# Optimization experiments

Hardware: AMD Instinct MI355X
Metric: run time of the kernel (lower is better)

## Reference

```python
import jax, jax.numpy as jnp
import numpy as np

B, P, C, WIN = 64, 24, 40, 64          # batch, acoustic params, phoneme classes, window
L1 = WIN - 4                            # after conv k=5: 60
L2 = L1 - 4                             # after primary conv k=5: 56
R = P * L2                              # num_routes = 24*56 = 1344
IC, OC = 32, 16                         # capsule in/out channels
NUM_ITERS = 3


def squash(x, axis=-1):
    sq = jnp.sum(x * x, axis=axis, keepdims=True)
    return (sq / (1.0 + sq)) * x / (jnp.sqrt(sq) + 1e-8)


def conv1d(x, w, b):
    # x: (B, Cin, L), w: (Cout, Cin, K)
    out = jax.lax.conv_general_dilated(x, w, (1,), 'VALID',
                                       dimension_numbers=('NCH', 'OIH', 'NCH'))
    return out + b[None, :, None]


def batchnorm(x, g, b):
    # training-mode BN over (batch, length) per channel; x: (B, Ch, L)
    m = jnp.mean(x, axis=(0, 2), keepdims=True)
    v = jnp.var(x, axis=(0, 2), keepdims=True)
    return g[None, :, None] * (x - m) / jnp.sqrt(v + 1e-5) + b[None, :, None]


def setup_inputs() -> dict:
    key = jax.random.key(0)
    ks = jax.random.split(key, 12)
    d = {}
    d['x'] = jax.random.normal(ks[0], (B, WIN, P), dtype=jnp.float32)
    # project: Conv1d(24 -> 256, k=5) + BN(256)
    d['conv1_w'] = jax.random.normal(ks[1], (256, P, 5), dtype=jnp.float32) * (1.0 / np.sqrt(P * 5))
    d['conv1_b'] = jnp.zeros((256,), dtype=jnp.float32)
    d['bn1_g'] = jnp.ones((256,), dtype=jnp.float32)
    d['bn1_b'] = jnp.zeros((256,), dtype=jnp.float32)
    d['prim_w'] = jax.random.normal(ks[2], (P * 32, 256, 5), dtype=jnp.float32) * (1.0 / np.sqrt(256 * 5))
    d['prim_b'] = jnp.zeros((P * 32,), dtype=jnp.float32)
    d['bn2_g'] = jnp.ones((32,), dtype=jnp.float32)
    d['bn2_b'] = jnp.zeros((32,), dtype=jnp.float32)
    # digit capsule routing weights (1, C, R, 16, 32) as in torch (randn)
    d['W_cap'] = jax.random.normal(ks[3], (1, C, R, OC, IC), dtype=jnp.float32) * 0.05
    # classifier: Linear(16*C -> 256), Linear(256 -> C)
    d['cls_w1'] = jax.random.normal(ks[4], (256, OC * C), dtype=jnp.float32) * (1.0 / np.sqrt(OC * C))
    d['cls_b1'] = jnp.zeros((256,), dtype=jnp.float32)
    d['cls_w2'] = jax.random.normal(ks[5], (C, 256), dtype=jnp.float32) * (1.0 / np.sqrt(256))
    d['cls_b2'] = jnp.zeros((C,), dtype=jnp.float32)
    d['dec_w1'] = jax.random.normal(ks[6], (256, OC * C), dtype=jnp.float32) * (1.0 / np.sqrt(OC * C))
    d['dec_b1'] = jnp.zeros((256,), dtype=jnp.float32)
    d['dec_w2'] = jax.random.normal(ks[7], (WIN * P, 256), dtype=jnp.float32) * (1.0 / np.sqrt(256))
    d['dec_b2'] = jnp.zeros((WIN * P,), dtype=jnp.float32)
    return d


def reference(x, conv1_w, conv1_b, bn1_g, bn1_b, prim_w, prim_b, bn2_g, bn2_b,
              W_cap, cls_w1, cls_b1, cls_w2, cls_b2, dec_w1, dec_b1, dec_w2, dec_b2):
    h = jax.nn.relu(batchnorm(conv1d(jnp.transpose(x, (0, 2, 1)), conv1_w, conv1_b), bn1_g, bn1_b))
    # primary capsules: fused conv -> (B, 24*32, 56); capsule i occupies length slice i
    u = conv1d(h, prim_w, prim_b)                       # (B, 768, 56)
    u = u.reshape(B, P, 32, L2).transpose(0, 2, 1, 3).reshape(B, 32, R)  # concat along length dim
    u = batchnorm(u, bn2_g, bn2_b)
    u = squash(jnp.transpose(u, (0, 2, 1)), axis=-1)    # (B, R, 32)
    # digit capsule: u_hat = W @ x  -> (B, C, R, 16)
    u_hat = jnp.einsum('crdi,bri->bcrd', W_cap[0], u)
    # dynamic routing
    b_ij = jnp.zeros((B, C, R, 1), dtype=u_hat.dtype)
    for it in range(NUM_ITERS):
        c_ij = jax.nn.softmax(b_ij, axis=1)             # softmax over capsules
        s_j = jnp.sum(c_ij * u_hat, axis=2)             # (B, C, 16)
        v_j = squash(s_j, axis=-1)
        if it < NUM_ITERS - 1:
            a_ij = jnp.einsum('bcrd,bcd->bcr', u_hat, v_j)[..., None]
            b_ij = b_ij + a_ij
    flat = v_j.reshape(B, -1)                           # (B, 640)
    logits = jax.nn.relu(flat @ cls_w1.T + cls_b1) @ cls_w2.T + cls_b2
    pred_y = jax.nn.softmax(logits, axis=-1)
    # y is None branch: one-hot of argmax
    y = jax.nn.one_hot(jnp.argmax(pred_y, axis=1), C, dtype=v_j.dtype)
    masked = (v_j * y[:, :, None]).reshape(B, -1)
    pred_x = jax.nn.sigmoid(jax.nn.relu(masked @ dec_w1.T + dec_b1) @ dec_w2.T + dec_b2)
    pred_x = pred_x.reshape(B, WIN, P)
    return (pred_x, pred_y)
```

## Files before the change

### kernel.cpp

```cpp
#include <hip/hip_runtime.h>
#include <math.h>

#define BB_ 64
#define P_  24
#define C_  40
#define WIN_ 64
#define L1_ 60
#define L2_ 56
#define R_  1344

#define O_USQ   0ull
#define O_UHAT  2752512ull
#define O_H     30277632ull
#define O_HB    3735552ull
#define O_WT    4227072ull
#define O_UP    25755648ull
#define O_STATS 57802752ull
#define O_A1    57803328ull
#define O_B1S   57803584ull
#define O_A2    57803840ull
#define O_B2S   57803872ull
#define O_S     57803904ull
#define O_V     57967744ull
#define WS_FLOATS_NEEDED 58008704ull

typedef short bf16x8 __attribute__((ext_vector_type(8)));
typedef float f32x4 __attribute__((ext_vector_type(4)));

__device__ __forceinline__ float dot4f(float4 a, float4 b) {
    return a.x*b.x + a.y*b.y + a.z*b.z + a.w*b.w;
}

__device__ __forceinline__ unsigned short f2bf(float x) {
    unsigned int u = __float_as_uint(x);
    u += 0x7fffu + ((u >> 16) & 1u);
    return (unsigned short)(u >> 16);
}
__device__ __forceinline__ float bfl(unsigned int u) {
    return __uint_as_float(u << 16);
}
__device__ __forceinline__ float bfh(unsigned int u) {
    return __uint_as_float(u & 0xffff0000u);
}

__global__ void k0w(const float* __restrict__ w2, unsigned short* __restrict__ wt) {
    int o2 = blockIdx.x, t = threadIdx.x;
    const float* src = &w2[(size_t)o2 * 1280 + t * 5];
    #pragma unroll
    for (int kt = 0; kt < 5; kt++)
        wt[((size_t)kt * 768 + o2) * 256 + t] = f2bf(src[kt]);
}

__global__ void k1_conv1(const float* __restrict__ x, const float* __restrict__ w1,
                         const float* __restrict__ c1b, float* __restrict__ h) {
    __shared__ float xs[24 * 20];
    __shared__ float wl[64 * 121];
    int t = threadIdx.x;
    int lq = blockIdx.x, b = blockIdx.y, ocg = blockIdx.z;
    for (int idx = t; idx < 456; idx += 256) {
        int p = idx / 19, tau = idx - p * 19;
        xs[p * 20 + tau] = x[b * 1536 + (lq * 15 + tau) * 24 + p];
    }
    for (int idx = t; idx < 7680; idx += 256) {
        int o_ = idx / 120, cix = idx - o_ * 120;
        wl[o_ * 121 + cix] = w1[(ocg * 64 + o_) * 120 + cix];
    }
    __syncthreads();
    int g = t >> 6;
    int ol = t & 63;
    int LV = (g < 3) ? 4 : 3;
    int o = ocg * 64 + ol;
    float acc[4] = {0.f, 0.f, 0.f, 0.f};
    for (int p = 0; p < 24; p++) {
        float4 xa = *(const float4*)&xs[p * 20 + g * 4];
        float4 xb = *(const float4*)&xs[p * 20 + g * 4 + 4];
        float xr[8] = {xa.x, xa.y, xa.z, xa.w, xb.x, xb.y, xb.z, xb.w};
        #pragma unroll
        for (int k = 0; k < 5; k++) {
            float w = wl[ol * 121 + p * 5 + k];
            #pragma unroll
            for (int li = 0; li < 4; li++) acc[li] += xr[li + k] * w;
        }
    }
    for (int li = 0; li < LV; li++) {
        int l = lq * 15 + g * 4 + li;
        h[(size_t)(b * 60 + l) * 256 + o] = acc[li] + c1b[o];
    }
}

__global__ void k2a(const float* __restrict__ h, float* __restrict__ sum1, float* __restrict__ ss1) {
    int t = threadIdx.x;
    float s = 0.f, q = 0.f;
    for (int i = 0; i < 64; i++) {
        float v = h[(size_t)(blockIdx.x * 64 + i) * 256 + t];
        s += v; q += v * v;
    }
    atomicAdd(&sum1[t], s);
    atomicAdd(&ss1[t], q);
}

__global__ void k2b(const float* __restrict__ sum1, const float* __restrict__ ss1,
                    const float* __restrict__ g, const float* __restrict__ be,
                    float* __restrict__ a1, float* __restrict__ b1s) {
    int o = threadIdx.x;
    float m = sum1[o] * (1.f / 3840.f);
    float v = ss1[o] * (1.f / 3840.f) - m * m;
    float a = g[o] / sqrtf(v + 1e-5f);
    a1[o] = a;
    b1s[o] = be[o] - m * a;
}

__global__ void k2c(const float* __restrict__ h, const float* __restrict__ a1,
                    const float* __restrict__ b1s, unsigned short* __restrict__ hb) {
    int gid = blockIdx.x * 256 + threadIdx.x;
    int base = gid * 4;
    int ic = base & 255;
    float4 v = *(const float4*)&h[base];
    float4 a = *(const float4*)&a1[ic];
    float4 bb = *(const float4*)&b1s[ic];
    unsigned int w0 = (unsigned int)f2bf(fmaxf(v.x * a.x + bb.x, 0.f))
                    | ((unsigned int)f2bf(fmaxf(v.y * a.y + bb.y, 0.f)) << 16);
    unsigned int w1 = (unsigned int)f2bf(fmaxf(v.z * a.z + bb.z, 0.f))
                    | ((unsigned int)f2bf(fmaxf(v.w * a.w + bb.w, 0.f)) << 16);
    uint2 o = {w0, w1};
    *(uint2*)&hb[base] = o;
}

__global__ __launch_bounds__(256) void k3_mfma(
        const unsigned short* __restrict__ hb, const unsigned short* __restrict__ wt,
        const float* __restrict__ pb, float* __restrict__ up) {
    __shared__ unsigned short hs[68 * 40];
    __shared__ unsigned short wsd[5 * 64 * 40];
    int t = threadIdx.x;
    int m0 = blockIdx.x * 64;
    int b = blockIdx.y;
    int wid = t >> 6, lane = t & 63;
    int wm = wid >> 1, wn = wid & 1;
    int ln = lane & 15, grp = lane >> 4;

    f32x4 acc[2][2];
    #pragma unroll
    for (int i = 0; i < 2; i++)
        #pragma unroll
        for (int j = 0; j < 2; j++) acc[i][j] = (f32x4){0.f, 0.f, 0.f, 0.f};

    for (int ic0 = 0; ic0 < 256; ic0 += 32) {
        __syncthreads();
        for (int idx = t; idx < 272; idx += 256) {
            int row = idx >> 2, q = idx & 3;
            int hrow = row < 60 ? row : 59;
            uint4 v = *(const uint4*)&hb[((size_t)b * 60 + hrow) * 256 + ic0 + q * 8];
            *(uint4*)&hs[row * 40 + q * 8] = v;
        }
        #pragma unroll
        for (int it = 0; it < 5; it++) {
            int idx = it * 256 + t;
            int row = idx >> 2, q = idx & 3;
            int kt = row >> 6, o2l = row & 63;
            uint4 v = *(const uint4*)&wt[((size_t)kt * 768 + m0 + o2l) * 256 + ic0 + q * 8];
            *(uint4*)&wsd[row * 40 + q * 8] = v;
        }
        __syncthreads();
        #pragma unroll
        for (int kt = 0; kt < 5; kt++) {
            bf16x8 af0 = *(const bf16x8*)&wsd[(kt * 64 + wm * 32 + ln) * 40 + grp * 8];
            bf16x8 af1 = *(const bf16x8*)&wsd[(kt * 64 + wm * 32 + 16 + ln) * 40 + grp * 8];
            bf16x8 bf0 = *(const bf16x8*)&hs[(wn * 32 + ln + kt) * 40 + grp * 8];
            bf16x8 bf1 = *(const bf16x8*)&hs[(wn * 32 + 16 + ln + kt) * 40 + grp * 8];
            acc[0][0] = __builtin_amdgcn_mfma_f32_16x16x32_bf16(af0, bf0, acc[0][0], 0, 0, 0);
            acc[0][1] = __builtin_amdgcn_mfma_f32_16x16x32_bf16(af0, bf1, acc[0][1], 0, 0, 0);
            acc[1][0] = __builtin_amdgcn_mfma_f32_16x16x32_bf16(af1, bf0, acc[1][0], 0, 0, 0);
            acc[1][1] = __builtin_amdgcn_mfma_f32_16x16x32_bf16(af1, bf1, acc[1][1], 0, 0, 0);
        }
    }
    #pragma unroll
    for (int ms = 0; ms < 2; ms++) {
        int o2 = m0 + wm * 32 + ms * 16 + grp * 4;
        float4 pv = *(const float4*)&pb[o2];
        #pragma unroll
        for (int ns = 0; ns < 2; ns++) {
            int l = wn * 32 + ns * 16 + ln;
            if (l < 56) {
                float4 v;
                v.x = acc[ms][ns][0] + pv.x;
                v.y = acc[ms][ns][1] + pv.y;
                v.z = acc[ms][ns][2] + pv.z;
                v.w = acc[ms][ns][3] + pv.w;
                *(float4*)&up[(size_t)b * 43008 + (size_t)l * 768 + o2] = v;
            }
        }
    }
}

__global__ void k4s(const float* __restrict__ up, float* __restrict__ sum2, float* __restrict__ ss2) {
    __shared__ float rs[256], rq[256];
    int t = threadIdx.x;
    float s = 0.f, q = 0.f;
    for (int i = 0; i < 32; i++) {
        size_t row = (size_t)(blockIdx.x * 32 + i) * 768;
        for (int c0 = 0; c0 < 768; c0 += 256) {
            float v = up[row + c0 + t];
            s += v; q += v * v;
        }
    }
    rs[t] = s; rq[t] = q;
    __syncthreads();
    if (t < 32) {
        float S = 0.f, Q = 0.f;
        for (int g2 = 0; g2 < 8; g2++) { S += rs[t + 32 * g2]; Q += rq[t + 32 * g2]; }
        atomicAdd(&sum2[t], S);
        atomicAdd(&ss2[t], Q);
    }
}

__global__ void k4b(const float* __restrict__ sum2, const float* __restrict__ ss2,
                    const float* __restrict__ g, const float* __restrict__ be,
                    float* __restrict__ a2, float* __restrict__ b2s) {
    int j = threadIdx.x;
    if (j >= 32) return;
    float m = sum2[j] * (1.f / 86016.f);
    float v = ss2[j] * (1.f / 86016.f) - m * m;
    float a = g[j] / sqrtf(v + 1e-5f);
    a2[j] = a;
    b2s[j] = be[j] - m * a;
}

__global__ void k5(const float* __restrict__ up, const float* __restrict__ a2,
                   const float* __restrict__ b2s, float* __restrict__ usq) {
    int t = threadIdx.x;
    int row = blockIdx.x * 8 + (t >> 5);
    int j = t & 31;
    int b = row / 1344, r = row - b * 1344;
    int p = r / 56, l = r - p * 56;
    float v = up[(size_t)b * 43008 + (size_t)l * 768 + p * 32 + j];
    float xv = a2[j] * v + b2s[j];
    float sq = xv * xv;
    #pragma unroll
    for (int m = 16; m >= 1; m >>= 1) sq += __shfl_xor(sq, m, 32);
    float scale = (sq / (1.f + sq)) / (sqrtf(sq) + 1e-8f);
    usq[(size_t)row * 32 + j] = xv * scale;
}

__global__ __launch_bounds__(256) void k6_uhat(const float* __restrict__ usq,
                                               const float* __restrict__ W,
                                               unsigned short* __restrict__ uhb) {
    __shared__ float us[64 * 36];
    __shared__ float wl[128 * 36];
    int t = threadIdx.x;
    int cdt = blockIdx.x, r = blockIdx.y;

    #pragma unroll
    for (int q = 0; q < 2; q++) {
        int idx4 = q * 256 + t;
        int b = idx4 >> 3, i4 = idx4 & 7;
        float4 v = *(const float4*)&usq[(size_t)(b * 1344 + r) * 32 + i4 * 4];
        *(float4*)&us[b * 36 + i4 * 4] = v;
    }
    #pragma unroll
    for (int q = 0; q < 4; q++) {
        int idx4 = q * 256 + t;
        int c_l = idx4 >> 7;
        int rest4 = idx4 & 127;
        float4 v = *(const float4*)&W[(size_t)(cdt * 8 + c_l) * 688128ull +
                                      (size_t)r * 512 + rest4 * 4];
        int cd_l = c_l * 16 + (rest4 >> 3);
        int i4 = rest4 & 7;
        *(float4*)&wl[cd_l * 36 + i4 * 4] = v;
    }
    __syncthreads();

    int tb = t & 7, tcd = t >> 3;
    float acc[8][4];
    #pragma unroll
    for (int i = 0; i < 8; i++)
        #pragma unroll
        for (int j = 0; j < 4; j++) acc[i][j] = 0.f;

    #pragma unroll
    for (int k4 = 0; k4 < 8; k4++) {
        float4 wv[4], ub[8];
        #pragma unroll
        for (int j = 0; j < 4; j++)
            wv[j] = *(const float4*)&wl[(tcd * 4 + j) * 36 + k4 * 4];
        #pragma unroll
        for (int bj = 0; bj < 8; bj++)
            ub[bj] = *(const float4*)&us[(bj * 8 + tb) * 36 + k4 * 4];
        #pragma unroll
        for (int bj = 0; bj < 8; bj++)
            #pragma unroll
            for (int j = 0; j < 4; j++)
                acc[bj][j] += dot4f(ub[bj], wv[j]);
    }

    #pragma unroll
    for (int bj = 0; bj < 8; bj++) {
        int b = bj * 8 + tb;
        unsigned int lo = (unsigned int)f2bf(acc[bj][0]) | ((unsigned int)f2bf(acc[bj][1]) << 16);
        unsigned int hi = (unsigned int)f2bf(acc[bj][2]) | ((unsigned int)f2bf(acc[bj][3]) << 16);
        uint2 o = {lo, hi};
        *(uint2*)&uhb[(size_t)(b * 1344 + r) * 640 + cdt * 128 + tcd * 4] = o;
    }
}

template<int UNIFORM>
__global__ void k_route(const unsigned short* __restrict__ uhb, const float* __restrict__ vsum,
                        float* __restrict__ sout) {
    __shared__ float sl[2560];
    int t = threadIdx.x, wid = t >> 6, lane = t & 63;
    int b = blockIdx.y, rt = blockIdx.x;
    bool act = lane < 40;
    int c = act ? lane : 0;
    float4 vs0 = {0,0,0,0}, vs1 = vs0, vs2 = vs0, vs3 = vs0;
    if (UNIFORM == 0 && act) {
        const float4* vp = (const float4*)&vsum[b * 640 + c * 16];
        vs0 = vp[0]; vs1 = vp[1]; vs2 = vp[2]; vs3 = vp[3];
    }
    float4 ac0 = {0,0,0,0}, ac1 = ac0, ac2 = ac0, ac3 = ac0;
    for (int i = 0; i < 8; i++) {
        int r = rt * 32 + wid * 8 + i;
        const uint4* u4 = (const uint4*)&uhb[((size_t)(b * 1344 + r) * 40 + c) * 16];
        float4 a0 = {0,0,0,0}, a1 = a0, a2 = a0, a3 = a0;
        if (act) {
            uint4 q0 = u4[0], q1 = u4[1];
            a0.x = bfl(q0.x); a0.y = bfh(q0.x); a0.z = bfl(q0.y); a0.w = bfh(q0.y);
            a1.x = bfl(q0.z); a1.y = bfh(q0.z); a1.z = bfl(q0.w); a1.w = bfh(q0.w);
            a2.x = bfl(q1.x); a2.y = bfh(q1.x); a2.z = bfl(q1.y); a2.w = bfh(q1.y);
            a3.x = bfl(q1.z); a3.y = bfh(q1.z); a3.z = bfl(q1.w); a3.w = bfh(q1.w);
        }
        float w;
        if (UNIFORM) {
            w = 0.025f;
        } else {
            float dt = act ? (dot4f(a0, vs0) + dot4f(a1, vs1) + dot4f(a2, vs2) + dot4f(a3, vs3))
                           : -1e30f;
            float mx = dt;
            #pragma unroll
            for (int m2 = 32; m2 >= 1; m2 >>= 1) mx = fmaxf(mx, __shfl_xor(mx, m2));
            float e = act ? __expf(dt - mx) : 0.f;
            float se = e;
            #pragma unroll
            for (int m2 = 32; m2 >= 1; m2 >>= 1) se += __shfl_xor(se, m2);
            w = e / se;
        }
        ac0.x += w * a0.x; ac0.y += w * a0.y; ac0.z += w * a0.z; ac0.w += w * a0.w;
        ac1.x += w * a1.x; ac1.y += w * a1.y; ac1.z += w * a1.z; ac1.w += w * a1.w;
        ac2.x += w * a2.x; ac2.y += w * a2.y; ac2.z += w * a2.z; ac2.w += w * a2.w;
        ac3.x += w * a3.x; ac3.y += w * a3.y; ac3.z += w * a3.z; ac3.w += w * a3.w;
    }
    if (act) {
        float4* sp = (float4*)&sl[wid * 640 + c * 16];
        sp[0] = ac0; sp[1] = ac1; sp[2] = ac2; sp[3] = ac3;
    }
    __syncthreads();
    for (int jj = t; jj < 640; jj += 256)
        atomicAdd(&sout[b * 640 + jj], sl[jj] + sl[640 + jj] + sl[1280 + jj] + sl[1920 + jj]);
}

__global__ void k8(const float* __restrict__ sin, float* __restrict__ vout,
                   float* __restrict__ vsum, int addsum) {
    int t = threadIdx.x;
    int row = blockIdx.x * 16 + (t >> 4);
    int d = t & 15;
    float v = sin[row * 16 + d];
    float sq = v * v;
    #pragma unroll
    for (int m = 8; m >= 1; m >>= 1) sq += __shfl_xor(sq, m, 16);
    float scale = (sq / (1.f + sq)) / (sqrtf(sq) + 1e-8f);
    float o = v * scale;
    vout[row * 16 + d] = o;
    if (addsum) vsum[row * 16 + d] += o;
}

__global__ void k10_head(const float* __restrict__ v,
                         const float* __restrict__ cw1, const float* __restrict__ cb1,
                         const float* __restrict__ cw2, const float* __restrict__ cb2,
                         const float* __restrict__ dw1, const float* __restrict__ db1,
                         const float* __restrict__ dw2, const float* __restrict__ db2,
                         float* __restrict__ out) {
    __shared__ float flat[640], hidp[512], hid[256], hd[256], lgs[40];
    __shared__ float smx, ssum;
    __shared__ int chat;
    int t = threadIdx.x, b = blockIdx.x;
    for (int j = t; j < 640; j += 512) flat[j] = v[b * 640 + j];
    __syncthreads();
    int h = t & 255, half = t >> 8;
    {
        float a = 0.f;
        int j0 = half * 320;
        for (int j = j0; j < j0 + 320; j++) a += flat[j] * cw1[h * 640 + j];
        hidp[t] = a;
    }
    __syncthreads();
    if (t < 256) hid[t] = fmaxf(hidp[t] + hidp[t + 256] + cb1[t], 0.f);
    __syncthreads();
    if (t < 320) {
        int c = t >> 3, s = t & 7;
        float p = 0.f;
        int h0 = s * 32;
        for (int h2 = h0; h2 < h0 + 32; h2++) p += hid[h2] * cw2[c * 256 + h2];
        p += __shfl_xor(p, 1); p += __shfl_xor(p, 2); p += __shfl_xor(p, 4);
        if (s == 0) lgs[c] = p + cb2[c];
    }
    __syncthreads();
    if (t == 0) {
        float mx = lgs[0]; int am = 0;
        for (int c2 = 1; c2 < 40; c2++) if (lgs[c2] > mx) { mx = lgs[c2]; am = c2; }
        float se = 0.f;
        for (int c2 = 0; c2 < 40; c2++) se += __expf(lgs[c2] - mx);
        smx = mx; ssum = se; chat = am;
    }
    __syncthreads();
    if (t < 40) out[98304 + b * 40 + t] = __expf(lgs[t] - smx) / ssum;
    int cb = chat * 16;
    if (t < 256) {
        float ad = db1[t];
        for (int j = 0; j < 16; j++) ad += flat[cb + j] * dw1[t * 640 + cb + j];
        hd[t] = fmaxf(ad, 0.f);
    }
    __syncthreads();
    for (int o = t; o < 1536; o += 512) {
        float z = db2[o];
        for (int h2 = 0; h2 < 256; h2++) z += hd[h2] * dw2[o * 256 + h2];
        out[b * 1536 + o] = 1.f / (1.f + __expf(-z));
    }
}

extern "C" void kernel_launch(void* const* d_in, const int* in_sizes, int n_in,
                              void* d_out, int out_size, void* d_ws, size_t ws_size,
                              hipStream_t stream) {
    const float* x   = (const float*)d_in[0];
    const float* c1w = (const float*)d_in[1];
    const float* c1b = (const float*)d_in[2];
    const float* g1  = (const float*)d_in[3];
    const float* be1 = (const float*)d_in[4];
    const float* pw  = (const float*)d_in[5];
    const float* pb  = (const float*)d_in[6];
    const float* g2  = (const float*)d_in[7];
    const float* be2 = (const float*)d_in[8];
    const float* Wc  = (const float*)d_in[9];
    const float* cw1 = (const float*)d_in[10];
    const float* cb1 = (const float*)d_in[11];
    const float* cw2 = (const float*)d_in[12];
    const float* cb2 = (const float*)d_in[13];
    const float* dw1 = (const float*)d_in[14];
    const float* db1 = (const float*)d_in[15];
    const float* dw2 = (const float*)d_in[16];
    const float* db2 = (const float*)d_in[17];

    if (ws_size < WS_FLOATS_NEEDED * 4ull) return;

    float* ws  = (float*)d_ws;
    float* out = (float*)d_out;
    float* usq  = ws + O_USQ;
    unsigned short* uhb = (unsigned short*)(ws + O_UHAT);
    float* hpre = ws + O_H;
    unsigned short* hbb = (unsigned short*)(ws + O_HB);
    unsigned short* wtb = (unsigned short*)(ws + O_WT);
    float* up   = ws + O_UP;
    float* sum1 = ws + O_STATS;
    float* ss1  = sum1 + 256;
    float* sum2 = ss1 + 256;
    float* ss2  = sum2 + 32;
    float* a1  = ws + O_A1;
    float* b1s = ws + O_B1S;
    float* a2  = ws + O_A2;
    float* b2s = ws + O_B2S;
    float* s0   = ws + O_S;
    float* s1   = s0 + 40960;
    float* s2   = s1 + 40960;
    float* vsum = s2 + 40960;
    float* vbuf = ws + O_V;

    hipMemsetAsync(sum1, 0, 576 * sizeof(float), stream);
    hipMemsetAsync(s0, 0, 163840 * sizeof(float), stream);

    k0w<<<768, 256, 0, stream>>>(pw, wtb);
    k1_conv1<<<dim3(4, 64, 4), 256, 0, stream>>>(x, c1w, c1b, hpre);
    k2a<<<60, 256, 0, stream>>>(hpre, sum1, ss1);
    k2b<<<1, 256, 0, stream>>>(sum1, ss1, g1, be1, a1, b1s);
    k2c<<<960, 256, 0, stream>>>(hpre, a1, b1s, hbb);
    k3_mfma<<<dim3(12, 64), 256, 0, stream>>>(hbb, wtb, pb, up);
    k4s<<<112, 256, 0, stream>>>(up, sum2, ss2);
    k4b<<<1, 64, 0, stream>>>(sum2, ss2, g2, be2, a2, b2s);
    k5<<<10752, 256, 0, stream>>>(up, a2, b2s, usq);
    k6_uhat<<<dim3(5, 1344), 256, 0, stream>>>(usq, Wc, uhb);
    k_route<1><<<dim3(42, 64), 256, 0, stream>>>(uhb, nullptr, s0);
    k8<<<160, 256, 0, stream>>>(s0, vbuf, vsum, 1);
    k_route<0><<<dim3(42, 64), 256, 0, stream>>>(uhb, vsum, s1);
    k8<<<160, 256, 0, stream>>>(s1, vbuf, vsum, 1);
    k_route<0><<<dim3(42, 64), 256, 0, stream>>>(uhb, vsum, s2);
    k8<<<160, 256, 0, stream>>>(s2, vbuf, vsum, 0);
    k10_head<<<64, 512, 0, stream>>>(vbuf, cw1, cb1, cw2, cb2, dw1, db1, dw2, db2, out);
}
```

Baseline: 426.6 us.

## Split classifier/decoder head into three parallel kernels with float4 dot products

The single 64-block head kernel is replaced by three kernels. The first computes the classifier hidden layer over a 64x4 grid, the second computes logits, softmax and the masked decoder first layer, and the third computes the decoder output over a 64x24 grid. Each kernel reads weights as float4 with 4-way shuffle reductions, which gives much more parallelism than the serial per-thread loops over 640 and 256 elements. This costs two extra kernel launches and a workspace round trip for the intermediate activations. The intermediates use a workspace region inside the O_H area, which appears to be no longer live at that point.

```diff
diff --git a/kernel.cpp b/kernel.cpp
--- a/kernel.cpp
+++ b/kernel.cpp
@@ -15,6 +15,8 @@
 #define O_HB    3735552ull
 #define O_WT    4227072ull
 #define O_UP    25755648ull
+#define O_HID   31260672ull
+#define O_HD    31277056ull
 #define O_STATS 57802752ull
 #define O_A1    57803328ull
 #define O_B1S   57803584ull
@@ -371,33 +373,45 @@
     if (addsum) vsum[row * 16 + d] += o;
 }
 
-__global__ void k10_head(const float* __restrict__ v,
-                         const float* __restrict__ cw1, const float* __restrict__ cb1,
-                         const float* __restrict__ cw2, const float* __restrict__ cb2,
-                         const float* __restrict__ dw1, const float* __restrict__ db1,
-                         const float* __restrict__ dw2, const float* __restrict__ db2,
-                         float* __restrict__ out) {
-    __shared__ float flat[640], hidp[512], hid[256], hd[256], lgs[40];
+__global__ void k10a(const float* __restrict__ v, const float* __restrict__ cw1,
+                     const float* __restrict__ cb1, float* __restrict__ hid) {
+    __shared__ float flat[640];
+    int t = threadIdx.x;
+    int b = blockIdx.x, hq = blockIdx.y;
+    for (int j = t; j < 640; j += 256) flat[j] = v[b * 640 + j];
+    __syncthreads();
+    int h_l = t >> 2, s = t & 3;
+    int h = hq * 64 + h_l;
+    const float4* wr = (const float4*)&cw1[(size_t)h * 640 + s * 160];
+    float a = 0.f;
+    #pragma unroll
+    for (int u = 0; u < 40; u++) {
+        float4 w4 = wr[u];
+        float4 f4 = *(const float4*)&flat[s * 160 + u * 4];
+        a += dot4f(w4, f4);
+    }
+    a += __shfl_xor(a, 1);
+    a += __shfl_xor(a, 2);
+    if (s == 0) hid[b * 256 + h] = fmaxf(a + cb1[h], 0.f);
+}
+
+__global__ void k10bc(const float* __restrict__ v, const float* __restrict__ hid,
+                      const float* __restrict__ cw2, const float* __restrict__ cb2,
+                      const float* __restrict__ dw1, const float* __restrict__ db1,
+                      float* __restrict__ out, float* __restrict__ hd) {
+    __shared__ float hl[256], lgs[40], msk[16];
     __shared__ float smx, ssum;
     __shared__ int chat;
     int t = threadIdx.x, b = blockIdx.x;
-    for (int j = t; j < 640; j += 512) flat[j] = v[b * 640 + j];
-    __syncthreads();
-    int h = t & 255, half = t >> 8;
+    if (t < 256) hl[t] = hid[b * 256 + t];
+    __syncthreads();
     {
-        float a = 0.f;
-        int j0 = half * 320;
-        for (int j = j0; j < j0 + 320; j++) a += flat[j] * cw1[h * 640 + j];
-        hidp[t] = a;
-    }
-    __syncthreads();
-    if (t < 256) hid[t] = fmaxf(hidp[t] + hidp[t + 256] + cb1[t], 0.f);
-    __syncthreads();
-    if (t < 320) {
         int c = t >> 3, s = t & 7;
         float p = 0.f;
-        int h0 = s * 32;
-        for (int h2 = h0; h2 < h0 + 32; h2++) p += hid[h2] * cw2[c * 256 + h2];
+        const float4* w4 = (const float4*)&cw2[c * 256 + s * 32];
+        const float4* h4 = (const float4*)&hl[s * 32];
+        #pragma unroll
+        for (int u = 0; u < 8; u++) p += dot4f(w4[u], h4[u]);
         p += __shfl_xor(p, 1); p += __shfl_xor(p, 2); p += __shfl_xor(p, 4);
         if (s == 0) lgs[c] = p + cb2[c];
     }
@@ -411,18 +425,38 @@
     }
     __syncthreads();
     if (t < 40) out[98304 + b * 40 + t] = __expf(lgs[t] - smx) / ssum;
-    int cb = chat * 16;
+    if (t < 16) msk[t] = v[b * 640 + chat * 16 + t];
+    __syncthreads();
     if (t < 256) {
+        int cb = chat * 16;
         float ad = db1[t];
-        for (int j = 0; j < 16; j++) ad += flat[cb + j] * dw1[t * 640 + cb + j];
-        hd[t] = fmaxf(ad, 0.f);
-    }
-    __syncthreads();
-    for (int o = t; o < 1536; o += 512) {
-        float z = db2[o];
-        for (int h2 = 0; h2 < 256; h2++) z += hd[h2] * dw2[o * 256 + h2];
-        out[b * 1536 + o] = 1.f / (1.f + __expf(-z));
-    }
+        const float4* w4 = (const float4*)&dw1[(size_t)t * 640 + cb];
+        #pragma unroll
+        for (int u = 0; u < 4; u++) {
+            float4 m4 = *(const float4*)&msk[u * 4];
+            ad += dot4f(w4[u], m4);
+        }
+        hd[b * 256 + t] = fmaxf(ad, 0.f);
+    }
+}
+
+__global__ void k10d(const float* __restrict__ hd, const float* __restrict__ dw2,
+                     const float* __restrict__ db2, float* __restrict__ out) {
+    __shared__ float hl[256];
+    int t = threadIdx.x;
+    int b = blockIdx.x, ot = blockIdx.y;
+    if (t < 256) hl[t] = hd[b * 256 + t];
+    __syncthreads();
+    int o_l = t >> 2, s = t & 3;
+    int o = ot * 64 + o_l;
+    const float4* w4 = (const float4*)&dw2[(size_t)o * 256 + s * 64];
+    const float4* h4 = (const float4*)&hl[s * 64];
+    float z = 0.f;
+    #pragma unroll
+    for (int u = 0; u < 16; u++) z += dot4f(w4[u], h4[u]);
+    z += __shfl_xor(z, 1);
+    z += __shfl_xor(z, 2);
+    if (s == 0) out[b * 1536 + o] = 1.f / (1.f + __expf(-(z + db2[o])));
 }
 
 extern "C" void kernel_launch(void* const* d_in, const int* in_sizes, int n_in,
@@ -457,6 +491,8 @@
     unsigned short* hbb = (unsigned short*)(ws + O_HB);
     unsigned short* wtb = (unsigned short*)(ws + O_WT);
     float* up   = ws + O_UP;
+    float* hidb = ws + O_HID;
+    float* hdb  = ws + O_HD;
     float* sum1 = ws + O_STATS;
     float* ss1  = sum1 + 256;
     float* sum2 = ss1 + 256;
@@ -490,5 +526,7 @@
     k8<<<160, 256, 0, stream>>>(s1, vbuf, vsum, 1);
     k_route<0><<<dim3(42, 64), 256, 0, stream>>>(uhb, vsum, s2);
     k8<<<160, 256, 0, stream>>>(s2, vbuf, vsum, 0);
-    k10_head<<<64, 512, 0, stream>>>(vbuf, cw1, cb1, cw2, cb2, dw1, db1, dw2, db2, out);
-}
+    k10a<<<dim3(64, 4), 256, 0, stream>>>(vbuf, cw1, cb1, hidb);
+    k10bc<<<64, 320, 0, stream>>>(vbuf, hidb, cw2, cb2, dw1, db1, out, hdb);
+    k10d<<<dim3(64, 24), 256, 0, stream>>>(hdb, dw2, db2, out);
+}
```

New measurement: 381.5 us. -10.6%, faster.
